# Performance work log

Measured on AMD Instinct MI355X. Metric: run time of the kernel, lower is better.

Reference implementation:

```python
import jax, jax.numpy as jnp
import numpy as np

FRAME_LEN = 256
HOP = 128
T_WINDOW = 128
N_MELS = 64


def setup_inputs() -> dict:
    key = jax.random.key(0)
    x_raw = jax.random.normal(key, (32, 16, 160000), dtype=jnp.float32)
    return {"x_raw": x_raw}


def reference(x_raw):
    # TF stft with pad_end=True: num_frames = ceil(T / hop)
    t = x_raw.shape[-1]
    num_frames = -(-t // HOP)
    pad = (num_frames - 1) * HOP + FRAME_LEN - t
    xp = jnp.pad(x_raw, ((0, 0), (0, 0), (0, pad)))

    # periodic Hann window (tf.signal.hann_window default)
    n = jnp.arange(FRAME_LEN, dtype=jnp.float32)
    window = 0.5 - 0.5 * jnp.cos(2.0 * jnp.pi * n / FRAME_LEN)

    # frame all batch/sensor signals at once: [B, S, F, L]
    idx = jnp.arange(num_frames)[:, None] * HOP + jnp.arange(FRAME_LEN)[None, :]
    frames = xp[..., idx] * window

    # batched real FFT -> [B, S, F, FRAME_LEN//2 + 1]
    stft = jnp.fft.rfft(frames, n=FRAME_LEN, axis=-1)
    logmag = jnp.log(jnp.abs(stft) + 1e-9)
    norm = jnp.clip(logmag, -12.0, 12.0)

    # tf.image.resize bilinear (half-pixel centers, no antialias)
    B, S = norm.shape[0], norm.shape[1]
    out = jax.image.resize(norm, (B, S, T_WINDOW, N_MELS), method="bilinear", antialias=False)
    return jnp.clip(out, -12.0, 12.0)
```

## Files before the change

### kernel.cpp

```cpp
#include <hip/hip_runtime.h>
#include <math.h>

#define HOP     128
#define SIGLEN  160000
#define NITER   8
#define NWAVES  2048
#define TWO_PI  6.2831853071795864f

__device__ __forceinline__ float2 cmul(float2 a, float2 b) {
    return make_float2(a.x * b.x - a.y * b.y, a.x * b.y + a.y * b.x);
}
__device__ __forceinline__ float2 cmul_mi(float2 a) {
    return make_float2(a.y, -a.x);
}

__device__ __forceinline__ void r4(float2 a, float2 b, float2 c, float2 d,
                                   float2& y0, float2& y1, float2& y2, float2& y3) {
    float t0r = a.x + c.x, t0i = a.y + c.y;
    float t1r = a.x - c.x, t1i = a.y - c.y;
    float t2r = b.x + d.x, t2i = b.y + d.y;
    float t3r = b.x - d.x, t3i = b.y - d.y;
    y0 = make_float2(t0r + t2r, t0i + t2i);
    y2 = make_float2(t0r - t2r, t0i - t2i);
    y1 = make_float2(t1r + t3i, t1i - t3r);
    y3 = make_float2(t1r - t3i, t1i + t3r);
}

__device__ __forceinline__ void dft16(const float2* p, float2* q) {
    float2 u[4][4];
    #pragma unroll
    for (int b = 0; b < 4; ++b)
        r4(p[b], p[4 + b], p[8 + b], p[12 + b], u[0][b], u[1][b], u[2][b], u[3][b]);
    const float C  = 0.70710678118654752f;
    const float c1 = 0.92387953251128676f, s1 = 0.38268343236508977f;
    u[1][1] = cmul(u[1][1], make_float2(c1, -s1));
    u[2][1] = cmul(u[2][1], make_float2(C, -C));
    u[3][1] = cmul(u[3][1], make_float2(s1, -c1));
    u[1][2] = cmul(u[1][2], make_float2(C, -C));
    u[2][2] = cmul_mi(u[2][2]);
    u[3][2] = cmul(u[3][2], make_float2(-C, -C));
    u[1][3] = cmul(u[1][3], make_float2(s1, -c1));
    u[2][3] = cmul(u[2][3], make_float2(-C, -C));
    u[3][3] = cmul(u[3][3], make_float2(-c1, s1));
    #pragma unroll
    for (int c = 0; c < 4; ++c)
        r4(u[c][0], u[c][1], u[c][2], u[c][3], q[c], q[c + 4], q[c + 8], q[c + 12]);
}

__device__ __forceinline__ float2 unpack_log(float2 A, float2 B) {
    float f0r = 0.5f * (A.x + B.x), f0i = 0.5f * (A.y - B.y);
    float f1r = 0.5f * (A.y + B.y), f1i = 0.5f * (B.x - A.x);
    float l0 = 0.5f * __logf(f0r * f0r + f0i * f0i);
    float l1 = 0.5f * __logf(f1r * f1r + f1i * f1i);
    return make_float2(fminf(fmaxf(l0, -12.0f), 12.0f),
                       fminf(fmaxf(l1, -12.0f), 12.0f));
}

#define LDS_SYNC() do { \
    asm volatile("s_waitcnt lgkmcnt(0)" ::: "memory"); \
    __builtin_amdgcn_s_barrier(); \
} while (0)

__global__ __launch_bounds__(64) void spectro_kernel(const float* __restrict__ x,
                                                     float* __restrict__ out) {
    const int wv   = blockIdx.x;
    const int lane = threadIdx.x;
    const int row  = lane >> 4;
    const int n2   = lane & 15;

    __shared__ float2 lds[1092];
    float2* Lrow = lds + 273 * row;

    float  wtab[16];
    float2 tw[16];
    #pragma unroll
    for (int i = 0; i < 16; ++i) {
        wtab[i] = 0.5f - 0.5f * __cosf((float)(16 * i + n2) * (TWO_PI / 256.0f));
        float ang = (float)(n2 * i) * (TWO_PI / 256.0f);
        tw[i] = make_float2(__cosf(ang), -__sinf(ang));
    }

    auto base_ptr = [&](int gi) -> const float* {
        const int t = 4 * (gi & 31) + row;
        const float src_t = ((float)t + 0.5f) * (1250.0f / 128.0f) - 0.5f;
        const int t0 = (int)src_t;
        return x + (long)(gi >> 5) * SIGLEN + (long)t0 * HOP + n2;
    };

    int g = NITER * wv;

    float cur[24], nxt[24];
    {
        const float* p = base_ptr(g);
        #pragma unroll
        for (int k = 0; k < 24; ++k) cur[k] = p[16 * k];
    }

    for (int i = 0; i < NITER; ++i, ++g) {
        if (i + 1 < NITER) {
            const float* p = base_ptr(g + 1);
            #pragma unroll
            for (int k = 0; k < 24; ++k) nxt[k] = p[16 * k];
        }

        const int t = 4 * (g & 31) + row;
        const float src_t = ((float)t + 0.5f) * (1250.0f / 128.0f) - 0.5f;
        const float ft = src_t - (float)(int)src_t;

        float2 z[16];
        #pragma unroll
        for (int n1 = 0; n1 < 16; ++n1)
            z[n1] = make_float2(wtab[n1] * cur[n1], wtab[n1] * cur[n1 + 8]);

        float2 A[16];
        dft16(z, A);
        #pragma unroll
        for (int k1 = 1; k1 < 16; ++k1) A[k1] = cmul(A[k1], tw[k1]);

        #pragma unroll
        for (int k1 = 0; k1 < 16; ++k1) Lrow[17 * k1 + n2] = A[k1];
        LDS_SYNC();

        float2 B[16];
        #pragma unroll
        for (int j = 0; j < 16; ++j) B[j] = Lrow[17 * n2 + j];

        float2 X16[16];
        dft16(B, X16);
        LDS_SYNC();

        #pragma unroll
        for (int k2 = 0; k2 < 16; ++k2) Lrow[16 * k2 + n2] = X16[k2];
        LDS_SYNC();

        #pragma unroll
        for (int j = 0; j < 4; ++j) {
            const int m = 16 * j + n2;
            const float src_m = ((float)m + 0.5f) * (129.0f / 64.0f) - 0.5f;
            const int   m0 = (int)src_m;
            const float fm = src_m - (float)m0;
            float2 A0 = Lrow[m0];
            float2 A1 = Lrow[m0 + 1];
            float2 B0 = Lrow[(256 - m0) & 255];
            float2 B1 = Lrow[255 - m0];
            float2 L0 = unpack_log(A0, B0);
            float2 L1 = unpack_log(A1, B1);
            float va = L0.x * (1.0f - fm) + L1.x * fm;
            float vb = L0.y * (1.0f - fm) + L1.y * fm;
            float val = va * (1.0f - ft) + vb * ft;
            val = fminf(fmaxf(val, -12.0f), 12.0f);
            out[(long)(4 * g + row) * 64 + m] = val;
        }
        LDS_SYNC();

        #pragma unroll
        for (int k = 0; k < 24; ++k) cur[k] = nxt[k];
    }
}

extern "C" void kernel_launch(void* const* d_in, const int* in_sizes, int n_in,
                              void* d_out, int out_size, void* d_ws, size_t ws_size,
                              hipStream_t stream) {
    const float* x = (const float*)d_in[0];
    float* out = (float*)d_out;
    spectro_kernel<<<dim3(NWAVES), dim3(64), 0, stream>>>(x, out);
}
```

Baseline: 34.23 us.

## Drop register prefetch, halve twiddle tables, replace barriers with compiler fences

Doubles the grid and halves the per-block work, removing the double-buffered register prefetch of the next frame. The window and twiddle tables shrink to 8 entries, using the Hann symmetry and composing the upper twiddles from two multiplies. Barriers are replaced by compiler-only fences, relying on the single-wave block and in-order LDS ops. It adds a minimum-occupancy launch bound of 4. The aim is lower register pressure and higher occupancy so latency is hidden by other waves instead of explicit prefetch. The cost is extra multiplies and less per-wave load overlap.

Measured after the change: 34.16 us. About the same (-0.2%).

```diff
diff --git a/kernel.cpp b/kernel.cpp
--- a/kernel.cpp
+++ b/kernel.cpp
@@ -3,8 +3,8 @@
 
 #define HOP     128
 #define SIGLEN  160000
-#define NITER   8
-#define NWAVES  2048
+#define NWAVES  4096
+#define GITER   4
 #define TWO_PI  6.2831853071795864f
 
 __device__ __forceinline__ float2 cmul(float2 a, float2 b) {
@@ -56,13 +56,10 @@
                        fminf(fmaxf(l1, -12.0f), 12.0f));
 }
 
-#define LDS_SYNC() do { \
-    asm volatile("s_waitcnt lgkmcnt(0)" ::: "memory"); \
-    __builtin_amdgcn_s_barrier(); \
-} while (0)
+#define FENCE() asm volatile("" ::: "memory")
 
-__global__ __launch_bounds__(64) void spectro_kernel(const float* __restrict__ x,
-                                                     float* __restrict__ out) {
+__global__ __launch_bounds__(64, 4) void spectro_kernel(const float* __restrict__ x,
+                                                        float* __restrict__ out) {
     const int wv   = blockIdx.x;
     const int lane = threadIdx.x;
     const int row  = lane >> 4;
@@ -71,67 +68,57 @@
     __shared__ float2 lds[1092];
     float2* Lrow = lds + 273 * row;
 
-    float  wtab[16];
-    float2 tw[16];
+    float  wtab8[8];
+    float2 tw[8];
     #pragma unroll
-    for (int i = 0; i < 16; ++i) {
-        wtab[i] = 0.5f - 0.5f * __cosf((float)(16 * i + n2) * (TWO_PI / 256.0f));
-        float ang = (float)(n2 * i) * (TWO_PI / 256.0f);
+    for (int i = 0; i < 8; ++i) {
+        wtab8[i] = 0.5f - 0.5f * __cosf((float)(16 * i + n2) * (TWO_PI / 256.0f));
+        float ang = (float)(n2 * (i + 1)) * (TWO_PI / 256.0f);
         tw[i] = make_float2(__cosf(ang), -__sinf(ang));
     }
 
-    auto base_ptr = [&](int gi) -> const float* {
-        const int t = 4 * (gi & 31) + row;
+    #pragma unroll 1
+    for (int it = 0; it < GITER; ++it) {
+        const int g   = GITER * wv + it;
+        const int t   = 4 * (g & 31) + row;
+        const int sig = g >> 5;
         const float src_t = ((float)t + 0.5f) * (1250.0f / 128.0f) - 0.5f;
-        const int t0 = (int)src_t;
-        return x + (long)(gi >> 5) * SIGLEN + (long)t0 * HOP + n2;
-    };
+        const int   t0 = (int)src_t;
+        const float ft = src_t - (float)t0;
+        const float* xb = x + (long)sig * SIGLEN + (long)t0 * HOP + n2;
 
-    int g = NITER * wv;
-
-    float cur[24], nxt[24];
-    {
-        const float* p = base_ptr(g);
+        float cur[24];
         #pragma unroll
-        for (int k = 0; k < 24; ++k) cur[k] = p[16 * k];
-    }
-
-    for (int i = 0; i < NITER; ++i, ++g) {
-        if (i + 1 < NITER) {
-            const float* p = base_ptr(g + 1);
-            #pragma unroll
-            for (int k = 0; k < 24; ++k) nxt[k] = p[16 * k];
-        }
-
-        const int t = 4 * (g & 31) + row;
-        const float src_t = ((float)t + 0.5f) * (1250.0f / 128.0f) - 0.5f;
-        const float ft = src_t - (float)(int)src_t;
+        for (int k = 0; k < 24; ++k) cur[k] = xb[16 * k];
 
         float2 z[16];
         #pragma unroll
-        for (int n1 = 0; n1 < 16; ++n1)
-            z[n1] = make_float2(wtab[n1] * cur[n1], wtab[n1] * cur[n1 + 8]);
+        for (int n1 = 0; n1 < 16; ++n1) {
+            float w = (n1 < 8) ? wtab8[n1] : 1.0f - wtab8[n1 - 8];
+            z[n1] = make_float2(w * cur[n1], w * cur[n1 + 8]);
+        }
 
         float2 A[16];
         dft16(z, A);
         #pragma unroll
-        for (int k1 = 1; k1 < 16; ++k1) A[k1] = cmul(A[k1], tw[k1]);
+        for (int k1 = 1; k1 < 16; ++k1) {
+            if (k1 <= 8) A[k1] = cmul(A[k1], tw[k1 - 1]);
+            else         A[k1] = cmul(cmul(A[k1], tw[7]), tw[k1 - 9]);
+        }
 
         #pragma unroll
         for (int k1 = 0; k1 < 16; ++k1) Lrow[17 * k1 + n2] = A[k1];
-        LDS_SYNC();
-
+        FENCE();
         float2 B[16];
         #pragma unroll
         for (int j = 0; j < 16; ++j) B[j] = Lrow[17 * n2 + j];
+        FENCE();
 
         float2 X16[16];
         dft16(B, X16);
-        LDS_SYNC();
-
         #pragma unroll
         for (int k2 = 0; k2 < 16; ++k2) Lrow[16 * k2 + n2] = X16[k2];
-        LDS_SYNC();
+        FENCE();
 
         #pragma unroll
         for (int j = 0; j < 4; ++j) {
@@ -151,10 +138,7 @@
             val = fminf(fmaxf(val, -12.0f), 12.0f);
             out[(long)(4 * g + row) * 64 + m] = val;
         }
-        LDS_SYNC();
-
-        #pragma unroll
-        for (int k = 0; k < 24; ++k) cur[k] = nxt[k];
+        FENCE();
     }
 }
 
```
